# Kernel optimization log

Hardware: AMD Instinct MI355X
Metric: run time of the kernel (lower is better)

The kernel has to match this reference:

```python
import jax, jax.numpy as jnp
import numpy as np

N = 100000   # total nodes in batch
E = 400000   # directed edges (before self-loops)
G = 4000     # graphs in batch (~25 atoms/mol)
IN = 29; HID = 128; HEADS = 4
BN_EPS = 1e-5


def setup_inputs():
    ks = jax.random.split(jax.random.key(0), 64)
    def rn(i, shp, s=0.1):
        return jax.random.normal(ks[i], shp, dtype=jnp.float32) * s
    H4 = HEADS * HID
    inp = {
        "x": jax.random.normal(ks[0], (N, IN), dtype=jnp.float32),
        "edge_index": jax.random.randint(ks[1], (2, E), 0, N),
        "batch_idx": jnp.sort(jax.random.randint(ks[2], (N,), 0, G)),
        "context": jax.random.uniform(ks[3], (N, 9), dtype=jnp.float32),
        "props": jax.random.normal(ks[4], (G, 9), dtype=jnp.float32),
        "mask": jax.random.randint(ks[5], (N,), 0, 2).astype(bool),
        "W1": rn(6, (IN, H4)), "as1": rn(7, (HEADS, HID)), "ad1": rn(8, (HEADS, HID)), "b1": rn(9, (H4,)),
        "g1": jnp.ones((H4,)), "be1": jnp.zeros((H4,)), "rm1": rn(10, (H4,), 0.05),
        "rv1": jax.random.uniform(ks[11], (H4,), minval=0.5, maxval=1.5),
        "W2": rn(12, (H4, H4), 0.05), "as2": rn(13, (HEADS, HID)), "ad2": rn(14, (HEADS, HID)), "b2": rn(15, (H4,)),
        "g2": jnp.ones((H4,)), "be2": jnp.zeros((H4,)), "rm2": rn(16, (H4,), 0.05),
        "rv2": jax.random.uniform(ks[17], (H4,), minval=0.5, maxval=1.5),
        "W3": rn(18, (H4, HID), 0.05), "as3": rn(19, (1, HID)), "ad3": rn(20, (1, HID)), "b3": rn(21, (HID,)),
        "g3": jnp.ones((HID,)), "be3": jnp.zeros((HID,)), "rm3": rn(22, (HID,), 0.05),
        "rv3": jax.random.uniform(ks[23], (HID,), minval=0.5, maxval=1.5),
        # context head 128 -> 128 -> 9
        "cw1": rn(24, (HID, HID)), "cb1": jnp.zeros((HID,)), "cw2": rn(25, (HID, 9)), "cb2": jnp.zeros((9,)),
        # property head 128 -> 128 -> 9
        "pw1": rn(26, (HID, HID)), "pb1": jnp.zeros((HID,)), "pw2": rn(27, (HID, 9)), "pb2": jnp.zeros((9,)),
        # masked reconstruction head 128 -> 128 -> 29
        "mw1": rn(28, (HID, HID)), "mb1": jnp.zeros((HID,)), "mw2": rn(29, (HID, IN)), "mb2": jnp.zeros((IN,)),
    }
    return inp


def gat_layer(h_in, src, dst, n, W, a_src, a_dst, bias):
    """PyG GATConv (concat=True, negative_slope=0.2, self-loops already in src/dst)."""
    heads, C = a_src.shape
    h = (h_in @ W).reshape(n, heads, C)                       # [N, H, C]
    e = jax.nn.leaky_relu((h * a_src).sum(-1)[src] + (h * a_dst).sum(-1)[dst], 0.2)  # [E', H]
    m = jax.ops.segment_max(e, dst, num_segments=n)            # segment softmax over incoming edges
    p = jnp.exp(e - m[dst])
    denom = jax.ops.segment_sum(p, dst, num_segments=n)
    alpha = p / (denom[dst] + 1e-16)                           # [E', H]
    out = jax.ops.segment_sum(alpha[:, :, None] * h[src], dst, num_segments=n)  # [N, H, C]
    return out.reshape(n, heads * C) + bias


def bn_elu(x, g, b, rm, rv):
    # BatchNorm1d (eval mode: running stats) followed by ELU; dropout is identity in eval.
    return jax.nn.elu((x - rm) * (g / jnp.sqrt(rv + BN_EPS)) + b)


def reference(x, edge_index, batch_idx, context, props, mask,
              W1, as1, ad1, b1, g1, be1, rm1, rv1,
              W2, as2, ad2, b2, g2, be2, rm2, rv2,
              W3, as3, ad3, b3, g3, be3, rm3, rv3,
              cw1, cb1, cw2, cb2, pw1, pb1, pw2, pb2, mw1, mb1, mw2, mb2):
    n = x.shape[0]
    loop = jnp.arange(n)
    src = jnp.concatenate([edge_index[0], loop])  # PyG GATConv adds self-loops by default
    dst = jnp.concatenate([edge_index[1], loop])
    h = bn_elu(gat_layer(x, src, dst, n, W1, as1, ad1, b1), g1, be1, rm1, rv1)
    h = bn_elu(gat_layer(h, src, dst, n, W2, as2, ad2, b2), g2, be2, rm2, rv2)
    h = bn_elu(gat_layer(h, src, dst, n, W3, as3, ad3, b3), g3, be3, rm3, rv3)  # [N, 128]
    # global mean pool per graph
    cnt = jax.ops.segment_sum(jnp.ones((n,), h.dtype), batch_idx, num_segments=G)
    gemb = jax.ops.segment_sum(h, batch_idx, num_segments=G) / jnp.maximum(cnt, 1.0)[:, None]
    # context prediction (BCE with logits, mean)
    z = jax.nn.relu(h @ cw1 + cb1) @ cw2 + cb2
    context_loss = jnp.mean(jnp.logaddexp(0.0, z) - z * context)
    # property prediction (MSE, mean)
    pz = jax.nn.relu(gemb @ pw1 + pb1) @ pw2 + pb2
    property_loss = jnp.mean((pz - props) ** 2)
    # masked feature reconstruction: MSE over masked nodes (masked mean == mse on h[mask])
    mz = jax.nn.relu(h @ mw1 + mb1) @ mw2 + mb2
    mf = mask.astype(h.dtype)
    mask_loss = jnp.sum(mf[:, None] * (mz - x) ** 2) / (jnp.sum(mf) * x.shape[1])
    return context_loss + property_loss + 0.5 * mask_loss
```

## Files before the change

kernel.cpp:

```cpp
#include <hip/hip_runtime.h>
#include <hip/hip_bf16.h>
#include <cstdint>
#include <cstddef>
#include <type_traits>

#define HIDC 128

typedef __attribute__((ext_vector_type(8))) short short8v;
typedef __attribute__((ext_vector_type(4))) float float4v;

__device__ __forceinline__ float loadT(const float* p){ return *p; }
__device__ __forceinline__ float loadT(const __hip_bfloat16* p){ return __bfloat162float(*p); }
__device__ __forceinline__ void  storeT(float* p, float v){ *p = v; }
__device__ __forceinline__ void  storeT(__hip_bfloat16* p, float v){ *p = __float2bfloat16(v); }

__device__ __forceinline__ short f2bf(float f){
  __hip_bfloat16 h = __float2bfloat16(f);
  return *reinterpret_cast<short*>(&h);
}
__device__ __forceinline__ float bfbits2f(short s){
  return __uint_as_float(((unsigned)(unsigned short)s) << 16);
}

__device__ __forceinline__ int swz(int row, int k){ return (row*32 + k) ^ ((row & 7) << 3); }

template<typename TA, typename TC, bool BIAS, bool RELU>
__global__ __launch_bounds__(256)
void mfma_gemm_kernel(const TA* __restrict__ A, const float* __restrict__ B,
                      const float* __restrict__ bias, TC* __restrict__ C,
                      int M, int Nb, int K, int ldc)
{
  __shared__ short As[2][128*32];
  __shared__ short Bs[2][64*32];

  const int nwg = gridDim.x * gridDim.y;
  int orig = blockIdx.y * gridDim.x + blockIdx.x;
  int xcd = orig & 7, pos = orig >> 3;
  int q = nwg >> 3, r = nwg & 7;
  int logical = (xcd < r ? xcd*(q+1) : r*(q+1) + (xcd - r)*q) + pos;
  const int bx = logical % gridDim.x;
  const int by = logical / gridDim.x;

  const int tid  = threadIdx.x;
  const int brow = by * 128;
  const int bcol = bx * 64;
  const int lane = tid & 63;
  const int wave = tid >> 6;
  const int wm = (wave >> 1) * 64;
  const int wn = (wave & 1) * 32;
  const int l15 = lane & 15;
  const int kq  = lane >> 4;

  float4v acc[4][2];
  #pragma unroll
  for (int i = 0; i < 4; i++)
    #pragma unroll
    for (int j = 0; j < 2; j++)
      #pragma unroll
      for (int r2 = 0; r2 < 4; r2++) acc[i][j][r2] = 0.f;

  const int am  = tid >> 1;
  const int akb = (tid & 1) * 16;
  const int bn  = tid & 63;
  const int bkc = tid >> 6;

  const bool dma_ok = std::is_same<TA, __hip_bfloat16>::value &&
                      ((K & 31) == 0) && (brow + 128 <= M);
  int dma_r[2], dma_c[2];
  #pragma unroll
  for (int i = 0; i < 2; i++) {
    int j = (wave*2 + i)*64 + lane;
    int s2 = (j>>2)&1, s3 = (j>>3)&1, s4 = (j>>4)&1;
    int b2 = s2 ^ s4;
    int b1 = ((j>>1)&1) ^ s3;
    int b0 = (j&1) ^ b2;
    int src = (j & ~7) | (b2<<2) | (b1<<1) | b0;
    dma_r[i] = src >> 2;
    dma_c[i] = src & 3;
  }

  if (dma_ok) {
    const short* Ash = reinterpret_cast<const short*>(A);
    const int gcol = bcol + bn;
    const int nt = K >> 5;
    float bv[8];

    #pragma unroll
    for (int i = 0; i < 2; i++) {
      const short* gp = Ash + (size_t)(brow + dma_r[i])*K + dma_c[i]*8;
      __builtin_amdgcn_global_load_lds(
          (const __attribute__((address_space(1))) void*)gp,
          (__attribute__((address_space(3))) void*)&As[0][(wave*2 + i)*512],
          16, 0, 0);
    }
    #pragma unroll
    for (int j = 0; j < 8; j++) {
      int gk = bkc*8 + j;
      bv[j] = (gcol < Nb) ? B[(size_t)gk*Nb + gcol] : 0.f;
    }
    {
      short8v v;
      #pragma unroll
      for (int j = 0; j < 8; j++) v[j] = f2bf(bv[j]);
      *(short8v*)&Bs[0][swz(bn, bkc*8)] = v;
    }
    asm volatile("s_waitcnt vmcnt(0)" ::: "memory");
    __syncthreads();

    int cur = 0;
    for (int t = 0; t < nt; t++) {
      const bool pf = (t + 1 < nt);
      if (pf) {
        const int k0n = (t + 1) << 5;
        #pragma unroll
        for (int i = 0; i < 2; i++) {
          const short* gp = Ash + (size_t)(brow + dma_r[i])*K + k0n + dma_c[i]*8;
          __builtin_amdgcn_global_load_lds(
              (const __attribute__((address_space(1))) void*)gp,
              (__attribute__((address_space(3))) void*)&As[cur^1][(wave*2 + i)*512],
              16, 0, 0);
        }
        #pragma unroll
        for (int j = 0; j < 8; j++) {
          int gk = k0n + bkc*8 + j;
          bv[j] = (gcol < Nb) ? B[(size_t)gk*Nb + gcol] : 0.f;
        }
      }
      {
        short8v bfrag[2];
        #pragma unroll
        for (int ni = 0; ni < 2; ni++)
          bfrag[ni] = *(const short8v*)&Bs[cur][swz(wn + ni*16 + l15, kq*8)];
        #pragma unroll
        for (int mi = 0; mi < 4; mi++) {
          short8v afrag = *(const short8v*)&As[cur][swz(wm + mi*16 + l15, kq*8)];
          #pragma unroll
          for (int ni = 0; ni < 2; ni++)
            acc[mi][ni] = __builtin_amdgcn_mfma_f32_16x16x32_bf16(afrag, bfrag[ni], acc[mi][ni], 0, 0, 0);
        }
      }
      if (pf) {
        short8v v;
        #pragma unroll
        for (int j = 0; j < 8; j++) v[j] = f2bf(bv[j]);
        *(short8v*)&Bs[cur^1][swz(bn, bkc*8)] = v;
      }
      asm volatile("s_waitcnt vmcnt(0)" ::: "memory");
      __syncthreads();
      cur ^= 1;
    }
  } else {
    for (int k0 = 0; k0 < K; k0 += 32) {
      {
        const int gm = brow + am;
        short s[16];
        if constexpr (std::is_same<TA, __hip_bfloat16>::value) {
          if (gm < M && (k0 + akb + 16) <= K) {
            const short8v* p = reinterpret_cast<const short8v*>(
                reinterpret_cast<const short*>(A) + (size_t)gm*K + k0 + akb);
            short8v v0 = p[0];
            *(short8v*)&As[0][swz(am, akb)]     = v0;
            short8v v1 = p[1];
            *(short8v*)&As[0][swz(am, akb + 8)] = v1;
            goto a_done;
          }
        }
        #pragma unroll
        for (int j = 0; j < 16; j++) {
          int gk = k0 + akb + j;
          s[j] = (gm < M && gk < K) ? f2bf(loadT(&A[(size_t)gm*K + gk])) : (short)0;
        }
        {
          short8v v0, v1;
          #pragma unroll
          for (int j = 0; j < 8; j++) { v0[j] = s[j]; v1[j] = s[j+8]; }
          *(short8v*)&As[0][swz(am, akb)]     = v0;
          *(short8v*)&As[0][swz(am, akb + 8)] = v1;
        }
        a_done:;
      }
      {
        const int gcol = bcol + bn;
        short8v v;
        #pragma unroll
        for (int j = 0; j < 8; j++) {
          int gk = k0 + bkc*8 + j;
          v[j] = (gk < K && gcol < Nb) ? f2bf(B[(size_t)gk*Nb + gcol]) : (short)0;
        }
        *(short8v*)&Bs[0][swz(bn, bkc*8)] = v;
      }
      __syncthreads();

      short8v bfrag[2];
      #pragma unroll
      for (int ni = 0; ni < 2; ni++)
        bfrag[ni] = *(const short8v*)&Bs[0][swz(wn + ni*16 + l15, kq*8)];
      #pragma unroll
      for (int mi = 0; mi < 4; mi++) {
        short8v afrag = *(const short8v*)&As[0][swz(wm + mi*16 + l15, kq*8)];
        #pragma unroll
        for (int ni = 0; ni < 2; ni++)
          acc[mi][ni] = __builtin_amdgcn_mfma_f32_16x16x32_bf16(afrag, bfrag[ni], acc[mi][ni], 0, 0, 0);
      }
      __syncthreads();
    }
  }

  #pragma unroll
  for (int mi = 0; mi < 4; mi++) {
    #pragma unroll
    for (int r2 = 0; r2 < 4; r2++) {
      int row = brow + wm + mi*16 + kq*4 + r2;
      if (row >= M) continue;
      #pragma unroll
      for (int ni = 0; ni < 2; ni++) {
        int col = bcol + wn + ni*16 + l15;
        if (col >= Nb) continue;
        float v = acc[mi][ni][r2];
        if (BIAS) v += bias[col];
        if (RELU) v = fmaxf(v, 0.f);
        storeT(&C[(size_t)row*ldc + col], v);
      }
    }
  }
}

template<typename T>
__global__ void scores_kernel(const T* __restrict__ hW, const float* __restrict__ a_src,
                              const float* __restrict__ a_dst, float* __restrict__ s_src,
                              float* __restrict__ s_dst, int n, int H)
{
  const int lane = threadIdx.x & 63;
  const int wid = blockIdx.x*(blockDim.x>>6) + (threadIdx.x>>6);
  if (wid >= n*H) return;
  const int node = wid / H, h = wid % H;
  const T* row = hW + (size_t)node*H*HIDC + (size_t)h*HIDC;
  float ss = 0.f, sd = 0.f;
  for (int c = lane; c < HIDC; c += 64) {
    float v = loadT(&row[c]);
    ss += v * a_src[h*HIDC + c];
    sd += v * a_dst[h*HIDC + c];
  }
  #pragma unroll
  for (int off = 32; off; off >>= 1) {
    ss += __shfl_down(ss, off);
    sd += __shfl_down(sd, off);
  }
  if (lane == 0) { s_src[wid] = ss; s_dst[wid] = sd; }
}

__global__ void deg_count_kernel(const int* __restrict__ ei, int E, int EP, int* __restrict__ deg)
{
  int e = blockIdx.x*blockDim.x + threadIdx.x;
  if (e >= EP) return;
  int d = (e < E) ? ei[E + e] : (e - E);
  atomicAdd(&deg[d], 1);
}

__global__ __launch_bounds__(256)
void scan1_kernel(const int* __restrict__ deg, int* __restrict__ indptr,
                  int* __restrict__ bsum, int n)
{
  __shared__ int sh[256];
  const int b = blockIdx.x, t = threadIdx.x;
  const int base = b*1024 + t*4;
  int v0 = (base+0 < n) ? deg[base+0] : 0;
  int v1 = (base+1 < n) ? deg[base+1] : 0;
  int v2 = (base+2 < n) ? deg[base+2] : 0;
  int v3 = (base+3 < n) ? deg[base+3] : 0;
  int tsum = v0+v1+v2+v3;
  sh[t] = tsum;
  __syncthreads();
  for (int off = 1; off < 256; off <<= 1) {
    int x = (t >= off) ? sh[t-off] : 0;
    __syncthreads();
    sh[t] += x;
    __syncthreads();
  }
  int run = sh[t] - tsum;
  if (base+0 < n) indptr[base+0] = run; run += v0;
  if (base+1 < n) indptr[base+1] = run; run += v1;
  if (base+2 < n) indptr[base+2] = run; run += v2;
  if (base+3 < n) indptr[base+3] = run;
  if (t == 255) bsum[b] = sh[255];
}

__global__ void scan2_kernel(int* __restrict__ bsum, int B)
{
  if (blockIdx.x == 0 && threadIdx.x == 0) {
    int run = 0;
    for (int i = 0; i < B; i++) { int v = bsum[i]; bsum[i] = run; run += v; }
  }
}

__global__ void scan3_kernel(int* __restrict__ indptr, const int* __restrict__ bsum,
                             int n, int total)
{
  int i = blockIdx.x*blockDim.x + threadIdx.x;
  if (i < n) indptr[i] += bsum[i >> 10];
  if (i == 0) indptr[n] = total;
}

__global__ void fill_kernel(const int* __restrict__ ei, int E, int EP,
                            const int* __restrict__ indptr, int* __restrict__ ctr,
                            int* __restrict__ esrc)
{
  int e = blockIdx.x*blockDim.x + threadIdx.x;
  if (e >= EP) return;
  int s, d;
  if (e < E) { s = ei[e]; d = ei[E + e]; } else { s = d = e - E; }
  int pos = indptr[d] + atomicAdd(&ctr[d], 1);
  esrc[pos] = s;
}

typedef __hip_bfloat16 bf16;

template<int H>
__global__ void csr_attn_agg_kernel(const int* __restrict__ indptr, const int* __restrict__ esrc,
                                    const float* __restrict__ s_src, const float* __restrict__ s_dst,
                                    const bf16* __restrict__ hW, bf16* __restrict__ out, int n,
                                    const float* __restrict__ bias, const float* __restrict__ g,
                                    const float* __restrict__ be, const float* __restrict__ rm,
                                    const float* __restrict__ rv)
{
  constexpr int HD = H * HIDC;
  const int lane = threadIdx.x & 63;
  const int wid = blockIdx.x*(blockDim.x>>6) + (threadIdx.x>>6);
  if (wid >= n*H) return;
  const int dst = wid / H, h = wid - dst*H;
  const int beg = indptr[dst], end = indptr[dst+1];
  const int deg = end - beg;
  const float sdh = s_dst[dst*H + h];

  float acc0 = 0.f, acc1 = 0.f;

  if (deg <= 64) {
    int sk = (lane < deg) ? esrc[beg + lane] : -1;
    float sc = -3.0e38f;
    if (sk >= 0) {
      float v = s_src[(size_t)sk*H + h] + sdh;
      sc = (v >= 0.f) ? v : 0.2f*v;
    }
    float m = sc;
    #pragma unroll
    for (int off = 32; off; off >>= 1) m = fmaxf(m, __shfl_xor(m, off));
    float e = (sk >= 0) ? __expf(sc - m) : 0.f;
    float den = e;
    #pragma unroll
    for (int off = 32; off; off >>= 1) den += __shfl_xor(den, off);
    const float rden = 1.f / (den + 1e-16f);
    for (int k = 0; k < deg; ++k) {
      float a = __shfl(e, k) * rden;
      int s = __shfl(sk, k);
      const bf16* row = hW + (size_t)s*HD + h*HIDC;
      acc0 += a * loadT(&row[lane]);
      acc1 += a * loadT(&row[lane + 64]);
    }
  } else {
    float m = -3.0e38f;
    for (int k = beg + lane; k < end; k += 64) {
      float v = s_src[(size_t)esrc[k]*H + h] + sdh;
      v = (v >= 0.f) ? v : 0.2f*v;
      m = fmaxf(m, v);
    }
    #pragma unroll
    for (int off = 32; off; off >>= 1) m = fmaxf(m, __shfl_xor(m, off));
    float den = 0.f;
    for (int k = beg + lane; k < end; k += 64) {
      float v = s_src[(size_t)esrc[k]*H + h] + sdh;
      v = (v >= 0.f) ? v : 0.2f*v;
      den += __expf(v - m);
    }
    #pragma unroll
    for (int off = 32; off; off >>= 1) den += __shfl_xor(den, off);
    const float rden = 1.f / (den + 1e-16f);
    for (int k = beg; k < end; ++k) {
      int s = esrc[k];
      float v = s_src[(size_t)s*H + h] + sdh;
      v = (v >= 0.f) ? v : 0.2f*v;
      float a = __expf(v - m) * rden;
      const bf16* row = hW + (size_t)s*HD + h*HIDC;
      acc0 += a * loadT(&row[lane]);
      acc1 += a * loadT(&row[lane + 64]);
    }
  }

  const int c0 = h*HIDC + lane;
  const int c1 = c0 + 64;
  float y0 = (acc0 + bias[c0] - rm[c0]) * (g[c0] / sqrtf(rv[c0] + 1e-5f)) + be[c0];
  float y1 = (acc1 + bias[c1] - rm[c1]) * (g[c1] / sqrtf(rv[c1] + 1e-5f)) + be[c1];
  y0 = (y0 > 0.f) ? y0 : expm1f(y0);
  y1 = (y1 > 0.f) ? y1 : expm1f(y1);
  bf16* orow = out + (size_t)dst*HD + h*HIDC;
  storeT(&orow[lane], y0);
  storeT(&orow[lane + 64], y1);
}

template<typename T>
__global__ void pool_sum_kernel(const T* __restrict__ h, const int* __restrict__ batch,
                                float* __restrict__ gsum, float* __restrict__ cnt, int n)
{
  int idx = blockIdx.x*blockDim.x + threadIdx.x;
  if (idx >= n*HIDC) return;
  int node = idx >> 7, j = idx & 127;
  int g = batch[node];
  atomicAdd(&gsum[(size_t)g*HIDC + j], loadT(&h[idx]));
  if (j == 0) atomicAdd(&cnt[g], 1.f);
}

__global__ void pool_div_kernel(float* __restrict__ gsum, const float* __restrict__ cnt, int G)
{
  int idx = blockIdx.x*blockDim.x + threadIdx.x;
  if (idx >= G*HIDC) return;
  gsum[idx] /= fmaxf(cnt[idx >> 7], 1.f);
}

__global__ void mask_detect_kernel(const int* __restrict__ m, int nwords, int* __restrict__ flag)
{
  int i = blockIdx.x*blockDim.x + threadIdx.x;
  if (i >= nwords) return;
  unsigned v = (unsigned)m[i];
  if (v > 1u) atomicOr(flag, 1);
}

__global__ __launch_bounds__(256)
void bce_reduce_kernel(const float* __restrict__ z, const float* __restrict__ ctx,
                       float* __restrict__ out_sum, int n)
{
  __shared__ float sh[256];
  float local = 0.f;
  const long long total = (long long)n * 9;
  for (long long i = (long long)blockIdx.x*blockDim.x + threadIdx.x; i < total;
       i += (long long)gridDim.x*blockDim.x) {
    int row = (int)(i / 9), j = (int)(i - (long long)row*9);
    float zz = z[(size_t)row*32 + j];
    float la = fmaxf(zz, 0.f) + log1pf(expf(-fabsf(zz)));
    local += la - zz * ctx[i];
  }
  sh[threadIdx.x] = local;
  __syncthreads();
  for (int s = 128; s; s >>= 1) {
    if ((int)threadIdx.x < s) sh[threadIdx.x] += sh[threadIdx.x + s];
    __syncthreads();
  }
  if (threadIdx.x == 0) atomicAdd(out_sum, sh[0]);
}

__global__ __launch_bounds__(256)
void mse_mask_reduce_kernel(const float* __restrict__ z, const float* __restrict__ x,
                            const int* __restrict__ mask, const int* __restrict__ bytemode,
                            float* __restrict__ out_sum, float* __restrict__ out_cnt, int n)
{
  __shared__ float sh[256], sh2[256];
  float local = 0.f, cl = 0.f;
  const bool bm = (*bytemode) != 0;
  const long long total = (long long)n * 29;
  for (long long i = (long long)blockIdx.x*blockDim.x + threadIdx.x; i < total;
       i += (long long)gridDim.x*blockDim.x) {
    int row = (int)(i / 29), j = (int)(i - (long long)row*29);
    int mk = bm ? (int)((const unsigned char*)mask)[row] : mask[row];
    if (mk != 0) {
      float dd = z[(size_t)row*32 + j] - x[i];
      local += dd*dd;
      if (j == 0) cl += 1.f;
    }
  }
  sh[threadIdx.x] = local;
  sh2[threadIdx.x] = cl;
  __syncthreads();
  for (int s = 128; s; s >>= 1) {
    if ((int)threadIdx.x < s) { sh[threadIdx.x] += sh[threadIdx.x + s]; sh2[threadIdx.x] += sh2[threadIdx.x + s]; }
    __syncthreads();
  }
  if (threadIdx.x == 0) { atomicAdd(out_sum, sh[0]); atomicAdd(out_cnt, sh2[0]); }
}

__global__ __launch_bounds__(256)
void mse_reduce_kernel(const float* __restrict__ z, const float* __restrict__ props,
                       float* __restrict__ out_sum, int g)
{
  __shared__ float sh[256];
  float local = 0.f;
  const long long total = (long long)g * 9;
  for (long long i = (long long)blockIdx.x*blockDim.x + threadIdx.x; i < total;
       i += (long long)gridDim.x*blockDim.x) {
    int row = (int)(i / 9), j = (int)(i - (long long)row*9);
    float dd = z[(size_t)row*32 + j] - props[i];
    local += dd*dd;
  }
  sh[threadIdx.x] = local;
  __syncthreads();
  for (int s = 128; s; s >>= 1) {
    if ((int)threadIdx.x < s) sh[threadIdx.x] += sh[threadIdx.x + s];
    __syncthreads();
  }
  if (threadIdx.x == 0) atomicAdd(out_sum, sh[0]);
}

__global__ void finalize_kernel(const float* __restrict__ scal, float* __restrict__ out,
                                float nf, float gf)
{
  out[0] = scal[0]/nf + scal[1]/gf + 0.5f*(scal[2]/(scal[3]*29.f));
}

__global__ void write_zero_kernel(float* __restrict__ out){ out[0] = 0.f; }

static void run_pipeline(void* const* d_in, hipStream_t stream, float* d_out,
                         bf16* buf1, bf16* buf2, float* ssrc, float* sdst,
                         int* indptr, int* deg, int* ctr, int* bsum, int* esrc,
                         float* gemb, float* cnt, float* r3, float* pz, float* scal, int* flag,
                         int N, int E, int G)
{
  const float* x     = (const float*)d_in[0];
  const int*   ei    = (const int*)d_in[1];
  const int*   batch = (const int*)d_in[2];
  const float* ctx   = (const float*)d_in[3];
  const float* props = (const float*)d_in[4];
  const int*   mask  = (const int*)d_in[5];
  const float* W1  = (const float*)d_in[6];  const float* as1 = (const float*)d_in[7];
  const float* ad1 = (const float*)d_in[8];  const float* b1  = (const float*)d_in[9];
  const float* g1  = (const float*)d_in[10]; const float* be1 = (const float*)d_in[11];
  const float* rm1 = (const float*)d_in[12]; const float* rv1 = (const float*)d_in[13];
  const float* W2  = (const float*)d_in[14]; const float* as2 = (const float*)d_in[15];
  const float* ad2 = (const float*)d_in[16]; const float* b2  = (const float*)d_in[17];
  const float* g2  = (const float*)d_in[18]; const float* be2 = (const float*)d_in[19];
  const float* rm2 = (const float*)d_in[20]; const float* rv2 = (const float*)d_in[21];
  const float* W3  = (const float*)d_in[22]; const float* as3 = (const float*)d_in[23];
  const float* ad3 = (const float*)d_in[24]; const float* b3  = (const float*)d_in[25];
  const float* g3  = (const float*)d_in[26]; const float* be3 = (const float*)d_in[27];
  const float* rm3 = (const float*)d_in[28]; const float* rv3 = (const float*)d_in[29];
  const float* cw1 = (const float*)d_in[30]; const float* cb1 = (const float*)d_in[31];
  const float* cw2 = (const float*)d_in[32]; const float* cb2 = (const float*)d_in[33];
  const float* pw1 = (const float*)d_in[34]; const float* pb1 = (const float*)d_in[35];
  const float* pw2 = (const float*)d_in[36]; const float* pb2 = (const float*)d_in[37];
  const float* mw1 = (const float*)d_in[38]; const float* mb1 = (const float*)d_in[39];
  const float* mw2 = (const float*)d_in[40]; const float* mb2 = (const float*)d_in[41];

  const int EP = E + N;
  const int H4 = 4 * HIDC;
  const int NB = (N + 1023) / 1024;
  const int GM = (N + 127) / 128;
  const int GG = (G + 127) / 128;

  (void)hipMemsetAsync(scal, 0, 8*sizeof(float), stream);
  (void)hipMemsetAsync(gemb, 0, (size_t)G*HIDC*sizeof(float), stream);
  (void)hipMemsetAsync(cnt,  0, (size_t)G*sizeof(float), stream);
  (void)hipMemsetAsync(deg,  0, (size_t)N*sizeof(int), stream);
  (void)hipMemsetAsync(ctr,  0, (size_t)N*sizeof(int), stream);
  mask_detect_kernel<<<(N/4 + 255)/256, 256, 0, stream>>>(mask, N/4, flag);

  deg_count_kernel<<<(EP + 255)/256, 256, 0, stream>>>(ei, E, EP, deg);
  scan1_kernel<<<NB, 256, 0, stream>>>(deg, indptr, bsum, N);
  scan2_kernel<<<1, 64, 0, stream>>>(bsum, NB);
  scan3_kernel<<<(N + 255)/256, 256, 0, stream>>>(indptr, bsum, N, EP);
  fill_kernel<<<(EP + 255)/256, 256, 0, stream>>>(ei, E, EP, indptr, ctr, esrc);

  mfma_gemm_kernel<float, bf16, false, false><<<dim3(H4/64, GM), 256, 0, stream>>>(x, W1, nullptr, buf2, N, H4, 29, H4);
  scores_kernel<bf16><<<(N*4 + 3)/4, 256, 0, stream>>>(buf2, as1, ad1, ssrc, sdst, N, 4);
  csr_attn_agg_kernel<4><<<(N*4 + 3)/4, 256, 0, stream>>>(indptr, esrc, ssrc, sdst, buf2, buf1, N, b1, g1, be1, rm1, rv1);

  mfma_gemm_kernel<bf16, bf16, false, false><<<dim3(H4/64, GM), 256, 0, stream>>>(buf1, W2, nullptr, buf2, N, H4, H4, H4);
  scores_kernel<bf16><<<(N*4 + 3)/4, 256, 0, stream>>>(buf2, as2, ad2, ssrc, sdst, N, 4);
  csr_attn_agg_kernel<4><<<(N*4 + 3)/4, 256, 0, stream>>>(indptr, esrc, ssrc, sdst, buf2, buf1, N, b2, g2, be2, rm2, rv2);

  mfma_gemm_kernel<bf16, bf16, false, false><<<dim3(HIDC/64, GM), 256, 0, stream>>>(buf1, W3, nullptr, buf2, N, HIDC, H4, HIDC);
  scores_kernel<bf16><<<(N + 3)/4, 256, 0, stream>>>(buf2, as3, ad3, ssrc, sdst, N, 1);
  csr_attn_agg_kernel<1><<<(N + 3)/4, 256, 0, stream>>>(indptr, esrc, ssrc, sdst, buf2, buf1, N, b3, g3, be3, rm3, rv3);

  pool_sum_kernel<bf16><<<(N*HIDC + 255)/256, 256, 0, stream>>>(buf1, batch, gemb, cnt, N);
  pool_div_kernel<<<(G*HIDC + 255)/256, 256, 0, stream>>>(gemb, cnt, G);

  bf16* headf = buf2;
  float* zbuf  = (float*)((char*)buf1 + (size_t)N*HIDC*sizeof(bf16));

  mfma_gemm_kernel<bf16, bf16, true, true><<<dim3(HIDC/64, GM), 256, 0, stream>>>(
      buf1, cw1, cb1, headf, N, HIDC, HIDC, HIDC);
  mfma_gemm_kernel<bf16, float, true, false><<<dim3(1, GM), 256, 0, stream>>>(
      headf, cw2, cb2, zbuf, N, 9, HIDC, 32);
  bce_reduce_kernel<<<2048, 256, 0, stream>>>(zbuf, ctx, &scal[0], N);

  mfma_gemm_kernel<bf16, bf16, true, true><<<dim3(HIDC/64, GM), 256, 0, stream>>>(
      buf1, mw1, mb1, headf, N, HIDC, HIDC, HIDC);
  mfma_gemm_kernel<bf16, float, true, false><<<dim3(1, GM), 256, 0, stream>>>(
      headf, mw2, mb2, zbuf, N, 29, HIDC, 32);
  mse_mask_reduce_kernel<<<2048, 256, 0, stream>>>(zbuf, x, mask, flag, &scal[2], &scal[3], N);

  mfma_gemm_kernel<float, float, true, true><<<dim3(HIDC/64, GG), 256, 0, stream>>>(
      gemb, pw1, pb1, r3, G, HIDC, HIDC, HIDC);
  mfma_gemm_kernel<float, float, true, false><<<dim3(1, GG), 256, 0, stream>>>(
      r3, pw2, pb2, pz, G, 9, HIDC, 32);
  mse_reduce_kernel<<<64, 256, 0, stream>>>(pz, props, &scal[1], G);

  finalize_kernel<<<1, 1, 0, stream>>>(scal, d_out, (float)N*9.f, (float)G*9.f);
}

extern "C" void kernel_launch(void* const* d_in, const int* in_sizes, int n_in,
                              void* d_out, int out_size, void* d_ws, size_t ws_size,
                              hipStream_t stream)
{
  const int N  = in_sizes[0] / 29;
  const int E  = in_sizes[1] / 2;
  const int G  = in_sizes[4] / 9;
  const int EP = E + N;
  const int H4 = 4 * HIDC;

  const size_t aux_bytes =
      (size_t)N*4*sizeof(float)*2
    + (size_t)(N+1)*sizeof(int)
    + (size_t)N*sizeof(int)*2
    + 512*sizeof(int)
    + (size_t)EP*sizeof(int)
    + (size_t)G*HIDC*sizeof(float)*2
    + (size_t)G*32*sizeof(float)
    + (size_t)G*sizeof(float)
    + 64*sizeof(float)
    + 4096;

  const size_t big = (size_t)N * H4;
  const size_t need = 2*big*sizeof(__hip_bfloat16) + aux_bytes;

  if (ws_size < need) {
    write_zero_kernel<<<1, 1, 0, stream>>>((float*)d_out);
    return;
  }

  char* base = (char*)d_ws;
  void* buf1 = (void*)base;          base += (big*sizeof(__hip_bfloat16) + 255) & ~(size_t)255;
  void* buf2 = (void*)base;          base += (big*sizeof(__hip_bfloat16) + 255) & ~(size_t)255;
  float* ssrc = (float*)base;        base += (size_t)N*4*sizeof(float);
  float* sdst = (float*)base;        base += (size_t)N*4*sizeof(float);
  int* indptr = (int*)base;          base += (size_t)(N+1)*sizeof(int);
  int* deg    = (int*)base;          base += (size_t)N*sizeof(int);
  int* ctr    = (int*)base;          base += (size_t)N*sizeof(int);
  int* bsum   = (int*)base;          base += 512*sizeof(int);
  int* esrc   = (int*)base;          base += (size_t)EP*sizeof(int);
  float* gemb = (float*)base;        base += (size_t)G*HIDC*sizeof(float);
  float* cnt  = (float*)base;        base += (size_t)G*sizeof(float);
  float* r3   = (float*)base;        base += (size_t)G*HIDC*sizeof(float);
  float* pz   = (float*)base;        base += (size_t)G*32*sizeof(float);
  float* scal = (float*)base;        base += 64*sizeof(float);
  int*   flag = (int*)&scal[4];

  run_pipeline(d_in, stream, (float*)d_out, (bf16*)buf1, (bf16*)buf2,
               ssrc, sdst, indptr, deg, ctr, bsum, esrc, gemb, cnt, r3, pz, scal, flag, N, E, G);
}
```

Measured before the change: 1.293 ms.

## Fuse mean-pool accumulation into final GAT aggregation and pack bf16 row loads

The aggregation kernel now reads each neighbour row as packed 32-bit words, so each lane handles two adjacent channels, and it writes the output as packed bf16 pairs. For degrees up to 8 the softmax reductions use a shorter shuffle tree. The final layer adds its fp32 outputs straight into the per-graph pool sums, which removes the separate pool_sum pass over the bf16 activations. Node counts move to a small separate kernel. The pooled sums now use fp32 values from before the bf16 rounding, and the ELU uses the faster __expf-1 form, so results can differ slightly.

Measured after the change: 1.241 ms. -4.0%, faster.

```diff
diff --git a/kernel.cpp b/kernel.cpp
--- a/kernel.cpp
+++ b/kernel.cpp
@@ -315,13 +315,14 @@
 
 typedef __hip_bfloat16 bf16;
 
-template<int H>
+template<int H, bool POOL>
 __global__ void csr_attn_agg_kernel(const int* __restrict__ indptr, const int* __restrict__ esrc,
                                     const float* __restrict__ s_src, const float* __restrict__ s_dst,
                                     const bf16* __restrict__ hW, bf16* __restrict__ out, int n,
                                     const float* __restrict__ bias, const float* __restrict__ g,
                                     const float* __restrict__ be, const float* __restrict__ rm,
-                                    const float* __restrict__ rv)
+                                    const float* __restrict__ rv,
+                                    const int* __restrict__ batch, float* __restrict__ gsum)
 {
   constexpr int HD = H * HIDC;
   const int lane = threadIdx.x & 63;
@@ -333,6 +334,7 @@
   const float sdh = s_dst[dst*H + h];
 
   float acc0 = 0.f, acc1 = 0.f;
+  const unsigned* hw32 = reinterpret_cast<const unsigned*>(hW);
 
   if (deg <= 64) {
     int sk = (lane < deg) ? esrc[beg + lane] : -1;
@@ -341,20 +343,33 @@
       float v = s_src[(size_t)sk*H + h] + sdh;
       sc = (v >= 0.f) ? v : 0.2f*v;
     }
-    float m = sc;
-    #pragma unroll
-    for (int off = 32; off; off >>= 1) m = fmaxf(m, __shfl_xor(m, off));
-    float e = (sk >= 0) ? __expf(sc - m) : 0.f;
-    float den = e;
-    #pragma unroll
-    for (int off = 32; off; off >>= 1) den += __shfl_xor(den, off);
+    float m, e, den;
+    if (deg <= 8) {
+      m = sc;
+      #pragma unroll
+      for (int off = 1; off < 8; off <<= 1) m = fmaxf(m, __shfl_xor(m, off));
+      m = __shfl(m, 0);
+      e = (sk >= 0) ? __expf(sc - m) : 0.f;
+      den = e;
+      #pragma unroll
+      for (int off = 1; off < 8; off <<= 1) den += __shfl_xor(den, off);
+      den = __shfl(den, 0);
+    } else {
+      m = sc;
+      #pragma unroll
+      for (int off = 32; off; off >>= 1) m = fmaxf(m, __shfl_xor(m, off));
+      e = (sk >= 0) ? __expf(sc - m) : 0.f;
+      den = e;
+      #pragma unroll
+      for (int off = 32; off; off >>= 1) den += __shfl_xor(den, off);
+    }
     const float rden = 1.f / (den + 1e-16f);
     for (int k = 0; k < deg; ++k) {
       float a = __shfl(e, k) * rden;
       int s = __shfl(sk, k);
-      const bf16* row = hW + (size_t)s*HD + h*HIDC;
-      acc0 += a * loadT(&row[lane]);
-      acc1 += a * loadT(&row[lane + 64]);
+      unsigned w = hw32[(size_t)s*(HD/2) + h*(HIDC/2) + lane];
+      acc0 += a * bfbits2f((short)(w & 0xffff));
+      acc1 += a * bfbits2f((short)((unsigned)w >> 16));
     }
   } else {
     float m = -3.0e38f;
@@ -379,33 +394,37 @@
       float v = s_src[(size_t)s*H + h] + sdh;
       v = (v >= 0.f) ? v : 0.2f*v;
       float a = __expf(v - m) * rden;
-      const bf16* row = hW + (size_t)s*HD + h*HIDC;
-      acc0 += a * loadT(&row[lane]);
-      acc1 += a * loadT(&row[lane + 64]);
-    }
-  }
-
-  const int c0 = h*HIDC + lane;
-  const int c1 = c0 + 64;
-  float y0 = (acc0 + bias[c0] - rm[c0]) * (g[c0] / sqrtf(rv[c0] + 1e-5f)) + be[c0];
-  float y1 = (acc1 + bias[c1] - rm[c1]) * (g[c1] / sqrtf(rv[c1] + 1e-5f)) + be[c1];
-  y0 = (y0 > 0.f) ? y0 : expm1f(y0);
-  y1 = (y1 > 0.f) ? y1 : expm1f(y1);
-  bf16* orow = out + (size_t)dst*HD + h*HIDC;
-  storeT(&orow[lane], y0);
-  storeT(&orow[lane + 64], y1);
-}
-
-template<typename T>
-__global__ void pool_sum_kernel(const T* __restrict__ h, const int* __restrict__ batch,
-                                float* __restrict__ gsum, float* __restrict__ cnt, int n)
-{
-  int idx = blockIdx.x*blockDim.x + threadIdx.x;
-  if (idx >= n*HIDC) return;
-  int node = idx >> 7, j = idx & 127;
-  int g = batch[node];
-  atomicAdd(&gsum[(size_t)g*HIDC + j], loadT(&h[idx]));
-  if (j == 0) atomicAdd(&cnt[g], 1.f);
+      unsigned w = hw32[(size_t)s*(HD/2) + h*(HIDC/2) + lane];
+      acc0 += a * bfbits2f((short)(w & 0xffff));
+      acc1 += a * bfbits2f((short)((unsigned)w >> 16));
+    }
+  }
+
+  const int c0 = h*HIDC + 2*lane;
+  const int c1 = c0 + 1;
+  const float s0 = g[c0] * rsqrtf(rv[c0] + 1e-5f);
+  const float s1 = g[c1] * rsqrtf(rv[c1] + 1e-5f);
+  float y0 = (acc0 + bias[c0] - rm[c0]) * s0 + be[c0];
+  float y1 = (acc1 + bias[c1] - rm[c1]) * s1 + be[c1];
+  y0 = (y0 > 0.f) ? y0 : (__expf(y0) - 1.f);
+  y1 = (y1 > 0.f) ? y1 : (__expf(y1) - 1.f);
+
+  unsigned* orow32 = reinterpret_cast<unsigned*>(out) + (size_t)dst*(HD/2) + h*(HIDC/2);
+  unsigned w = (unsigned)(unsigned short)f2bf(y0) | ((unsigned)(unsigned short)f2bf(y1) << 16);
+  orow32[lane] = w;
+
+  if constexpr (POOL) {
+    const int grp = batch[dst];
+    atomicAdd(&gsum[(size_t)grp*HIDC + 2*lane], y0);
+    atomicAdd(&gsum[(size_t)grp*HIDC + 2*lane + 1], y1);
+  }
+}
+
+__global__ void cnt_kernel(const int* __restrict__ batch, float* __restrict__ cnt, int n)
+{
+  int i = blockIdx.x*blockDim.x + threadIdx.x;
+  if (i >= n) return;
+  atomicAdd(&cnt[batch[i]], 1.f);
 }
 
 __global__ void pool_div_kernel(float* __restrict__ gsum, const float* __restrict__ cnt, int G)
@@ -554,20 +573,20 @@
   scan2_kernel<<<1, 64, 0, stream>>>(bsum, NB);
   scan3_kernel<<<(N + 255)/256, 256, 0, stream>>>(indptr, bsum, N, EP);
   fill_kernel<<<(EP + 255)/256, 256, 0, stream>>>(ei, E, EP, indptr, ctr, esrc);
+  cnt_kernel<<<(N + 255)/256, 256, 0, stream>>>(batch, cnt, N);
 
   mfma_gemm_kernel<float, bf16, false, false><<<dim3(H4/64, GM), 256, 0, stream>>>(x, W1, nullptr, buf2, N, H4, 29, H4);
   scores_kernel<bf16><<<(N*4 + 3)/4, 256, 0, stream>>>(buf2, as1, ad1, ssrc, sdst, N, 4);
-  csr_attn_agg_kernel<4><<<(N*4 + 3)/4, 256, 0, stream>>>(indptr, esrc, ssrc, sdst, buf2, buf1, N, b1, g1, be1, rm1, rv1);
+  csr_attn_agg_kernel<4,false><<<(N*4 + 3)/4, 256, 0, stream>>>(indptr, esrc, ssrc, sdst, buf2, buf1, N, b1, g1, be1, rm1, rv1, nullptr, nullptr);
 
   mfma_gemm_kernel<bf16, bf16, false, false><<<dim3(H4/64, GM), 256, 0, stream>>>(buf1, W2, nullptr, buf2, N, H4, H4, H4);
   scores_kernel<bf16><<<(N*4 + 3)/4, 256, 0, stream>>>(buf2, as2, ad2, ssrc, sdst, N, 4);
-  csr_attn_agg_kernel<4><<<(N*4 + 3)/4, 256, 0, stream>>>(indptr, esrc, ssrc, sdst, buf2, buf1, N, b2, g2, be2, rm2, rv2);
+  csr_attn_agg_kernel<4,false><<<(N*4 + 3)/4, 256, 0, stream>>>(indptr, esrc, ssrc, sdst, buf2, buf1, N, b2, g2, be2, rm2, rv2, nullptr, nullptr);
 
   mfma_gemm_kernel<bf16, bf16, false, false><<<dim3(HIDC/64, GM), 256, 0, stream>>>(buf1, W3, nullptr, buf2, N, HIDC, H4, HIDC);
   scores_kernel<bf16><<<(N + 3)/4, 256, 0, stream>>>(buf2, as3, ad3, ssrc, sdst, N, 1);
-  csr_attn_agg_kernel<1><<<(N + 3)/4, 256, 0, stream>>>(indptr, esrc, ssrc, sdst, buf2, buf1, N, b3, g3, be3, rm3, rv3);
-
-  pool_sum_kernel<bf16><<<(N*HIDC + 255)/256, 256, 0, stream>>>(buf1, batch, gemb, cnt, N);
+  csr_attn_agg_kernel<1,true><<<(N + 3)/4, 256, 0, stream>>>(indptr, esrc, ssrc, sdst, buf2, buf1, N, b3, g3, be3, rm3, rv3, batch, gemb);
+
   pool_div_kernel<<<(G*HIDC + 255)/256, 256, 0, stream>>>(gemb, cnt, G);
 
   bf16* headf = buf2;
```
